# Performance work log

Measured on AMD Instinct MI355X. Metric: run time of the kernel, lower is better.

The kernel has to match this reference:

```python
import math
import jax, jax.numpy as jnp
import numpy as np

INPUT_DIM = 1024
OUTPUT_DIM = 1024
DEGREE = 8
EPS = 1.0


def setup_inputs() -> dict:
    key = jax.random.key(0)
    k1, k2 = jax.random.split(key)
    x = jax.random.normal(k1, (8192, INPUT_DIM), dtype=jnp.float32)
    std = 1.0 / (INPUT_DIM * (DEGREE + 1))
    hermite_coeffs = std * jax.random.normal(k2, (INPUT_DIM, OUTPUT_DIM, DEGREE + 1), dtype=jnp.float32)
    return {"x": x, "hermite_coeffs": hermite_coeffs}


def _hermite_basis(x):
    # x: [B, I] squashed input; returns [B, I, DEGREE+1] Hermite-function basis.
    pi_q = math.pi ** (-0.25)
    gauss = jnp.exp(-0.5 * x * x)
    h0 = pi_q * gauss
    hs = [h0]
    if DEGREE > 0:
        hs.append(math.sqrt(2.0) * pi_q * x * gauss)
    for i in range(2, DEGREE + 1):
        hs.append(math.sqrt(2.0 / i) * x * hs[i - 1] - math.sqrt((i - 1) / i) * hs[i - 2])
    return jnp.stack(hs, axis=-1)


def reference(x, hermite_coeffs):
    x = x.reshape(-1, INPUT_DIM)
    x = jnp.tanh(x) * (math.sqrt(2 * DEGREE + 1) + EPS)
    hermite = _hermite_basis(x)  # [B, I, D+1]
    y = jnp.einsum('bid,iod->bo', hermite, hermite_coeffs)
    return y.reshape(-1, OUTPUT_DIM)
```

## Files before the change

kernel.cpp:

```cpp
#include <hip/hip_runtime.h>

#define MDIM 8192
#define IDIM 1024
#define ODIM 1024
#define D1   9
#define KDIM (IDIM * D1)

typedef _Float16 half8   __attribute__((ext_vector_type(8)));
typedef _Float16 half2v  __attribute__((ext_vector_type(2)));
typedef float    float4v __attribute__((ext_vector_type(4)));

#define BSCALE 256.0f
#define INV_BSCALE (1.0f / 256.0f)
#define USCALE 5.123105625617661f
#define H0C 0.7511255444649425f
#define SQRT2 1.4142135623730951f

__device__ __forceinline__ void hermite9(float xv, float h[D1]) {
    float ax = fabsf(xv);
    float t  = __expf(-2.0f * ax);
    float th = (1.0f - t) / (1.0f + t);
    th = copysignf(th, xv);
    float u = th * USCALE;
    float g = __expf(-0.5f * u * u);
    h[0] = H0C * g;
    h[1] = SQRT2 * H0C * u * g;
    const float c1[D1] = {0.f, 0.f, 1.0f, 0.8164965809277260f, 0.7071067811865476f,
                          0.6324555320336759f, 0.5773502691896258f, 0.5345224838248488f, 0.5f};
    const float c2[D1] = {0.f, 0.f, 0.7071067811865476f, 0.8164965809277260f, 0.8660254037844386f,
                          0.8944271909999159f, 0.9128709291752769f, 0.9258200997725514f, 0.9354143466934853f};
#pragma unroll
    for (int d = 2; d < D1; ++d) h[d] = c1[d] * u * h[d - 1] - c2[d] * h[d - 2];
}

__global__ __launch_bounds__(256) void prep_b(const float* __restrict__ C,
                                              _Float16* __restrict__ Bt) {
    __shared__ float lds[288 * 33];
    const int t  = threadIdx.x;
    const int ti = blockIdx.x & 31;
    const int to = blockIdx.x >> 5;
    const float* base = C + (size_t)ti * 32 * 9216 + (size_t)to * 32 * 9;
#pragma unroll
    for (int j = 0; j < 36; ++j) {
        int f   = t + 256 * j;
        int row = f / 288;
        int col = f - row * 288;
        lds[col * 33 + row] = base[(size_t)row * 9216 + col];
    }
    __syncthreads();
    _Float16* bb = Bt + (size_t)to * 32 * KDIM + ti * 32;
#pragma unroll
    for (int j = 0; j < 36; ++j) {
        int e   = t + 256 * j;
        int i   = e & 31;
        int odp = e >> 5;
        int ol  = odp / 9;
        int d   = odp - ol * 9;
        bb[(size_t)ol * KDIM + d * IDIM + i] = (_Float16)(lds[odp * 33 + i] * BSCALE);
    }
}

__global__ __launch_bounds__(256) void prep_u(const float* __restrict__ x,
                                              _Float16* __restrict__ U,
                                              _Float16* __restrict__ H0) {
    size_t t = (size_t)blockIdx.x * 256 + threadIdx.x;
    const float4* xp = (const float4*)(x + t * 8);
    float4 a0 = xp[0], a1 = xp[1];
    float xv[8] = {a0.x, a0.y, a0.z, a0.w, a1.x, a1.y, a1.z, a1.w};
    half8 uu, hh;
#pragma unroll
    for (int e = 0; e < 8; ++e) {
        float v  = xv[e];
        float t2 = __expf(-2.0f * fabsf(v));
        float th = (1.0f - t2) / (1.0f + t2);
        float u  = copysignf(th, v) * USCALE;
        float g  = __expf(-0.5f * u * u);
        uu[e] = (_Float16)u;
        hh[e] = (_Float16)(H0C * g);
    }
    *(half8*)(U  + t * 8) = uu;
    *(half8*)(H0 + t * 8) = hh;
}

__global__ __launch_bounds__(256, 2) void gemm_fused3(
    const _Float16* __restrict__ U,
    const _Float16* __restrict__ H0,
    const _Float16* __restrict__ Bt,
    float* __restrict__ out)
{
    const int tid = threadIdx.x;
    const int w = tid >> 6;
    const int l = tid & 63;
    const int bn = blockIdx.x;
    const int bm = blockIdx.y;

    __shared__ _Float16 As[128 * 64];
    __shared__ _Float16 Bs[3][128 * 64];

    const int lrow8 = l >> 3;
    const int kgrp  = (l & 7) ^ lrow8;
    const _Float16* Bg = Bt + ((size_t)(bn * 128 + w * 8 + lrow8) * KDIM + kgrp * 8);

    const int q   = l >> 4;
    const int m16 = l & 15;
    const int s3  = m16 & 7;
    const int wm  = w >> 1, wn = w & 1;

    const int r  = tid >> 1;
    const int ih = tid & 1;
    const int r7 = r & 7;
    const size_t urow = (((size_t)(bm * 128 + r)) << 10) + ih * 32;

    constexpr float c1a[D1] = {0.f, 0.f, 1.0f, 0.8164965809277260f, 0.7071067811865476f,
                               0.6324555320336759f, 0.5773502691896258f, 0.5345224838248488f, 0.5f};
    constexpr float c2a[D1] = {0.f, 0.f, 0.7071067811865476f, 0.8164965809277260f, 0.8660254037844386f,
                               0.8944271909999159f, 0.9128709291752769f, 0.9258200997725514f, 0.9354143466934853f};

    half2v u2[16], hA[16], hB[16], ht[16];
    half8  ub[4], hb[4];
    const half2v sq2 = half2v{(_Float16)SQRT2, (_Float16)SQRT2};

    _Float16* arow = &As[r * 64];
    auto writeA = [&](const half2v* hts) {
#pragma unroll
        for (int c = 0; c < 4; ++c) {
            int slot = (ih * 4 + c) ^ r7;
            half8 vv;
#pragma unroll
            for (int pp = 0; pp < 4; ++pp) {
                vv[2*pp+0] = hts[4*c+pp][0];
                vv[2*pp+1] = hts[4*c+pp][1];
            }
            *(half8*)(arow + slot * 8) = vv;
        }
    };

    float4v acc[4][4] = {};

    {
        const half8* up = (const half8*)(U  + urow);
        const half8* hp = (const half8*)(H0 + urow);
#pragma unroll
        for (int a = 0; a < 4; ++a) { ub[a] = up[a]; hb[a] = hp[a]; }
#pragma unroll
        for (int a = 0; a < 4; ++a)
#pragma unroll
            for (int b = 0; b < 4; ++b) {
                u2[4*a+b] = half2v{ub[a][2*b], ub[a][2*b+1]};
                hA[4*a+b] = half2v{hb[a][2*b], hb[a][2*b+1]};
            }
#pragma unroll
        for (int p = 0; p < 16; ++p) { hB[p] = sq2 * u2[p] * hA[p]; ht[p] = hB[p]; }
    }
#pragma unroll
    for (int rr = 0; rr < 4; ++rr)
        __builtin_amdgcn_global_load_lds(
            (const __attribute__((address_space(1))) void*)(Bg + (size_t)(rr * 32) * KDIM),
            (__attribute__((address_space(3))) void*)((char*)&Bs[0][0] + (rr * 4 + w) * 1024),
            16, 0, 0);
#pragma unroll
    for (int rr = 0; rr < 4; ++rr)
        __builtin_amdgcn_global_load_lds(
            (const __attribute__((address_space(1))) void*)(Bg + (size_t)(rr * 32) * KDIM + IDIM),
            (__attribute__((address_space(3))) void*)((char*)&Bs[1][0] + (rr * 4 + w) * 1024),
            16, 0, 0);
    writeA(hA);
    asm volatile("s_waitcnt vmcnt(4) lgkmcnt(0)" ::: "memory");
    __builtin_amdgcn_s_barrier();
    asm volatile("" ::: "memory");

    auto window = [&](int ib, int d, bool do_e, bool do_wa, bool do_uh,
                      bool do_dma, int waitN, bool do_sync2, bool do_sync1) {
        const int cbuf = d % 3;

        __builtin_amdgcn_s_setprio(1);
#pragma unroll
        for (int ko = 0; ko < 2; ++ko) {
            const int slot = (q + 4 * ko) ^ s3;
            half8 af[4], bf[4];
#pragma unroll
            for (int i = 0; i < 4; ++i) {
                af[i] = *(const half8*)&As[(wm * 64 + i * 16 + m16) * 64 + slot * 8];
                bf[i] = *(const half8*)&Bs[cbuf][(wn * 64 + i * 16 + m16) * 64 + slot * 8];
            }
#pragma unroll
            for (int i = 0; i < 4; ++i)
#pragma unroll
                for (int j = 0; j < 4; ++j)
                    acc[i][j] = __builtin_amdgcn_mfma_f32_16x16x32_f16(af[i], bf[j], acc[i][j], 0, 0, 0);
        }
        __builtin_amdgcn_s_setprio(0);

        half2v htn[16];
        if (do_e) {
            const int t2d = (d <= 6) ? (d + 2) : (d - 7);
            if (t2d == 0) {
#pragma unroll
                for (int a = 0; a < 4; ++a)
#pragma unroll
                    for (int b = 0; b < 4; ++b) {
                        u2[4*a+b]  = half2v{ub[a][2*b], ub[a][2*b+1]};
                        htn[4*a+b] = half2v{hb[a][2*b], hb[a][2*b+1]};
                    }
#pragma unroll
                for (int p = 0; p < 16; ++p) hB[p] = htn[p];
            } else if (t2d == 1) {
#pragma unroll
                for (int p = 0; p < 16; ++p) {
                    htn[p] = sq2 * u2[p] * hB[p];
                    hA[p] = hB[p]; hB[p] = htn[p];
                }
            } else {
                const half2v c1v = half2v{(_Float16)c1a[t2d], (_Float16)c1a[t2d]};
                const half2v c2v = half2v{(_Float16)c2a[t2d], (_Float16)c2a[t2d]};
#pragma unroll
                for (int p = 0; p < 16; ++p) {
                    half2v tt = u2[p] * hB[p];
                    htn[p] = c1v * tt - c2v * hA[p];
                    hA[p] = hB[p]; hB[p] = htn[p];
                }
            }
        }

        if (do_sync2) {
            asm volatile("s_waitcnt lgkmcnt(0)" ::: "memory");
            __builtin_amdgcn_s_barrier();
            asm volatile("" ::: "memory");
        }

        if (do_wa) writeA(ht);
        if (do_e) {
#pragma unroll
            for (int p = 0; p < 16; ++p) ht[p] = htn[p];
        }
        if (do_uh) {
            const half8* up = (const half8*)(U  + urow + (size_t)(ib + 1) * 64);
            const half8* hp = (const half8*)(H0 + urow + (size_t)(ib + 1) * 64);
#pragma unroll
            for (int a = 0; a < 4; ++a) { ub[a] = up[a]; hb[a] = hp[a]; }
        }
        if (do_dma) {
            const int nkoff = (d <= 6) ? ((d + 2) * IDIM + ib * 64)
                                       : ((d - 7) * IDIM + ib * 64 + 64);
            const int nbuf = (d + 2) % 3;
#pragma unroll
            for (int rr = 0; rr < 4; ++rr)
                __builtin_amdgcn_global_load_lds(
                    (const __attribute__((address_space(1))) void*)(Bg + (size_t)(rr * 32) * KDIM + nkoff),
                    (__attribute__((address_space(3))) void*)((char*)&Bs[nbuf][0] + (rr * 4 + w) * 1024),
                    16, 0, 0);
        }
        if (do_sync1) {
            if (waitN == 12)     asm volatile("s_waitcnt vmcnt(12) lgkmcnt(0)" ::: "memory");
            else if (waitN == 4) asm volatile("s_waitcnt vmcnt(4) lgkmcnt(0)" ::: "memory");
            else                 asm volatile("s_waitcnt vmcnt(0) lgkmcnt(0)" ::: "memory");
            __builtin_amdgcn_s_barrier();
            asm volatile("" ::: "memory");
        }
    };

    for (int ib = 0; ib < 15; ++ib) {
#pragma unroll
        for (int d = 0; d < D1; ++d)
            window(ib, d, true, true, (d == 6), true, (d == 6) ? 12 : 4, true, true);
    }
    {
#pragma unroll
        for (int d = 0; d < 6; ++d)
            window(15, d, true, true, false, true, 4, true, true);
        window(15, 6, true,  true,  false, true,  4, true, true);
        window(15, 7, false, true,  false, false, 0, true, true);
        window(15, 8, false, false, false, false, 0, false, false);
    }

#pragma unroll
    for (int i = 0; i < 4; ++i) {
        int row = bm * 128 + wm * 64 + i * 16 + q * 4;
#pragma unroll
        for (int j = 0; j < 4; ++j) {
            int col = bn * 128 + wn * 64 + j * 16 + m16;
            float* op = out + (size_t)row * ODIM + col;
#pragma unroll
            for (int r2 = 0; r2 < 4; ++r2)
                op[(size_t)r2 * ODIM] = acc[i][j][r2] * INV_BSCALE;
        }
    }
}

__global__ void naive_kernel(const float* __restrict__ x, const float* __restrict__ C,
                             float* __restrict__ out) {
    __shared__ float hb[IDIM * D1];
    int b = blockIdx.x;
    int tid = threadIdx.x;
    for (int i = tid; i < IDIM; i += 256) {
        float h[D1];
        hermite9(x[(size_t)b * IDIM + i], h);
#pragma unroll
        for (int d = 0; d < D1; ++d) hb[i * D1 + d] = h[d];
    }
    __syncthreads();
    for (int o = tid; o < ODIM; o += 256) {
        float acc = 0.f;
        for (int i = 0; i < IDIM; ++i) {
            const float* cp = C + ((size_t)i * ODIM + o) * D1;
            const float* hp = hb + i * D1;
#pragma unroll
            for (int d = 0; d < D1; ++d) acc += hp[d] * cp[d];
        }
        out[(size_t)b * ODIM + o] = acc;
    }
}

extern "C" void kernel_launch(void* const* d_in, const int* in_sizes, int n_in,
                              void* d_out, int out_size, void* d_ws, size_t ws_size,
                              hipStream_t stream) {
    const float* x      = (const float*)d_in[0];
    const float* coeffs = (const float*)d_in[1];
    float* out = (float*)d_out;

    const size_t bt_bytes = (size_t)ODIM * KDIM * sizeof(_Float16);
    const size_t u_bytes  = (size_t)MDIM * IDIM * sizeof(_Float16);

    if (ws_size >= bt_bytes + 2 * u_bytes) {
        _Float16* Bt = (_Float16*)d_ws;
        _Float16* Uv = (_Float16*)((char*)d_ws + bt_bytes);
        _Float16* H0 = (_Float16*)((char*)d_ws + bt_bytes + u_bytes);
        hipLaunchKernelGGL(prep_b, dim3(1024), dim3(256), 0, stream, coeffs, Bt);
        hipLaunchKernelGGL(prep_u, dim3((MDIM * IDIM) / 2048), dim3(256), 0, stream, x, Uv, H0);
        hipLaunchKernelGGL(gemm_fused3, dim3(8, 64), dim3(256), 0, stream, Uv, H0, Bt, out);
    } else {
        hipLaunchKernelGGL(naive_kernel, dim3(MDIM), dim3(256), 0, stream, x, coeffs, out);
    }
}
```

Baseline: 274.0 us.

## Build Hermite A-fragments in registers instead of staging them through LDS

```diff
diff --git a/kernel.cpp b/kernel.cpp
--- a/kernel.cpp
+++ b/kernel.cpp
@@ -50,13 +50,19 @@
     __syncthreads();
     _Float16* bb = Bt + (size_t)to * 32 * KDIM + ti * 32;
 #pragma unroll
-    for (int j = 0; j < 36; ++j) {
-        int e   = t + 256 * j;
-        int i   = e & 31;
-        int odp = e >> 5;
-        int ol  = odp / 9;
-        int d   = odp - ol * 9;
-        bb[(size_t)ol * KDIM + d * IDIM + i] = (_Float16)(lds[odp * 33 + i] * BSCALE);
+    for (int j = 0; j < 5; ++j) {
+        int s = t + 256 * j;
+        if (s < 1152) {
+            int i8  = s & 3;
+            int odp = s >> 2;
+            int ol  = odp / 9;
+            int d   = odp - ol * 9;
+            half8 vv;
+#pragma unroll
+            for (int e = 0; e < 8; ++e)
+                vv[e] = (_Float16)(lds[odp * 33 + i8 * 8 + e] * BSCALE);
+            *(half8*)(bb + (size_t)ol * KDIM + d * IDIM + i8 * 8) = vv;
+        }
     }
 }
 
@@ -82,7 +88,7 @@
     *(half8*)(H0 + t * 8) = hh;
 }
 
-__global__ __launch_bounds__(256, 2) void gemm_fused3(
+__global__ __launch_bounds__(256, 2) void gemm_fused4(
     const _Float16* __restrict__ U,
     const _Float16* __restrict__ H0,
     const _Float16* __restrict__ Bt,
@@ -94,7 +100,6 @@
     const int bn = blockIdx.x;
     const int bm = blockIdx.y;
 
-    __shared__ _Float16 As[128 * 64];
     __shared__ _Float16 Bs[3][128 * 64];
 
     const int lrow8 = l >> 3;
@@ -106,154 +111,96 @@
     const int s3  = m16 & 7;
     const int wm  = w >> 1, wn = w & 1;
 
-    const int r  = tid >> 1;
-    const int ih = tid & 1;
-    const int r7 = r & 7;
-    const size_t urow = (((size_t)(bm * 128 + r)) << 10) + ih * 32;
+    const size_t ubase = ((size_t)(bm * 128 + wm * 64 + m16)) << 10;
 
     constexpr float c1a[D1] = {0.f, 0.f, 1.0f, 0.8164965809277260f, 0.7071067811865476f,
                                0.6324555320336759f, 0.5773502691896258f, 0.5345224838248488f, 0.5f};
     constexpr float c2a[D1] = {0.f, 0.f, 0.7071067811865476f, 0.8164965809277260f, 0.8660254037844386f,
                                0.8944271909999159f, 0.9128709291752769f, 0.9258200997725514f, 0.9354143466934853f};
 
-    half2v u2[16], hA[16], hB[16], ht[16];
-    half8  ub[4], hb[4];
-    const half2v sq2 = half2v{(_Float16)SQRT2, (_Float16)SQRT2};
-
-    _Float16* arow = &As[r * 64];
-    auto writeA = [&](const half2v* hts) {
-#pragma unroll
-        for (int c = 0; c < 4; ++c) {
-            int slot = (ih * 4 + c) ^ r7;
-            half8 vv;
-#pragma unroll
-            for (int pp = 0; pp < 4; ++pp) {
-                vv[2*pp+0] = hts[4*c+pp][0];
-                vv[2*pp+1] = hts[4*c+pp][1];
+    half8 u8[8], hA8[8], hB8[8];
+
+    auto loadUH = [&](int ib) {
+        const int ibo = ib * 64;
+#pragma unroll
+        for (int i16 = 0; i16 < 4; ++i16)
+#pragma unroll
+            for (int ko = 0; ko < 2; ++ko) {
+                const size_t off = ubase + ((size_t)(i16 * 16) << 10) + ibo + (q + 4 * ko) * 8;
+                u8 [i16 * 2 + ko] = *(const half8*)(U  + off);
+                hA8[i16 * 2 + ko] = *(const half8*)(H0 + off);
             }
-            *(half8*)(arow + slot * 8) = vv;
-        }
     };
 
+    auto dmaB = [&](int nkoff, int nbuf) {
+#pragma unroll
+        for (int rr = 0; rr < 4; ++rr)
+            __builtin_amdgcn_global_load_lds(
+                (const __attribute__((address_space(1))) void*)(Bg + (size_t)(rr * 32) * KDIM + nkoff),
+                (__attribute__((address_space(3))) void*)((char*)&Bs[nbuf][0] + (rr * 4 + w) * 1024),
+                16, 0, 0);
+    };
+
     float4v acc[4][4] = {};
 
-    {
-        const half8* up = (const half8*)(U  + urow);
-        const half8* hp = (const half8*)(H0 + urow);
-#pragma unroll
-        for (int a = 0; a < 4; ++a) { ub[a] = up[a]; hb[a] = hp[a]; }
-#pragma unroll
-        for (int a = 0; a < 4; ++a)
-#pragma unroll
-            for (int b = 0; b < 4; ++b) {
-                u2[4*a+b] = half2v{ub[a][2*b], ub[a][2*b+1]};
-                hA[4*a+b] = half2v{hb[a][2*b], hb[a][2*b+1]};
-            }
-#pragma unroll
-        for (int p = 0; p < 16; ++p) { hB[p] = sq2 * u2[p] * hA[p]; ht[p] = hB[p]; }
-    }
-#pragma unroll
-    for (int rr = 0; rr < 4; ++rr)
-        __builtin_amdgcn_global_load_lds(
-            (const __attribute__((address_space(1))) void*)(Bg + (size_t)(rr * 32) * KDIM),
-            (__attribute__((address_space(3))) void*)((char*)&Bs[0][0] + (rr * 4 + w) * 1024),
-            16, 0, 0);
-#pragma unroll
-    for (int rr = 0; rr < 4; ++rr)
-        __builtin_amdgcn_global_load_lds(
-            (const __attribute__((address_space(1))) void*)(Bg + (size_t)(rr * 32) * KDIM + IDIM),
-            (__attribute__((address_space(3))) void*)((char*)&Bs[1][0] + (rr * 4 + w) * 1024),
-            16, 0, 0);
-    writeA(hA);
-    asm volatile("s_waitcnt vmcnt(4) lgkmcnt(0)" ::: "memory");
+    loadUH(0);
+    dmaB(0, 0);
+    dmaB(IDIM, 1);
+    asm volatile("s_waitcnt vmcnt(4)" ::: "memory");
     __builtin_amdgcn_s_barrier();
     asm volatile("" ::: "memory");
 
-    auto window = [&](int ib, int d, bool do_e, bool do_wa, bool do_uh,
-                      bool do_dma, int waitN, bool do_sync2, bool do_sync1) {
+    auto window = [&](int ib, int d, bool do_uh, bool do_dma, int waitN, bool do_sync) {
         const int cbuf = d % 3;
+
+        if (do_uh) loadUH(ib + 1);
 
         __builtin_amdgcn_s_setprio(1);
 #pragma unroll
         for (int ko = 0; ko < 2; ++ko) {
             const int slot = (q + 4 * ko) ^ s3;
-            half8 af[4], bf[4];
+            half8 bf[4];
+#pragma unroll
+            for (int j = 0; j < 4; ++j)
+                bf[j] = *(const half8*)&Bs[cbuf][(wn * 64 + j * 16 + m16) * 64 + slot * 8];
 #pragma unroll
             for (int i = 0; i < 4; ++i) {
-                af[i] = *(const half8*)&As[(wm * 64 + i * 16 + m16) * 64 + slot * 8];
-                bf[i] = *(const half8*)&Bs[cbuf][(wn * 64 + i * 16 + m16) * 64 + slot * 8];
+                half8 af = (d == 0) ? hA8[i * 2 + ko] : hB8[i * 2 + ko];
+#pragma unroll
+                for (int j = 0; j < 4; ++j)
+                    acc[i][j] = __builtin_amdgcn_mfma_f32_16x16x32_f16(af, bf[j], acc[i][j], 0, 0, 0);
             }
-#pragma unroll
-            for (int i = 0; i < 4; ++i)
-#pragma unroll
-                for (int j = 0; j < 4; ++j)
-                    acc[i][j] = __builtin_amdgcn_mfma_f32_16x16x32_f16(af[i], bf[j], acc[i][j], 0, 0, 0);
         }
         __builtin_amdgcn_s_setprio(0);
 
-        half2v htn[16];
-        if (do_e) {
-            const int t2d = (d <= 6) ? (d + 2) : (d - 7);
-            if (t2d == 0) {
-#pragma unroll
-                for (int a = 0; a < 4; ++a)
-#pragma unroll
-                    for (int b = 0; b < 4; ++b) {
-                        u2[4*a+b]  = half2v{ub[a][2*b], ub[a][2*b+1]};
-                        htn[4*a+b] = half2v{hb[a][2*b], hb[a][2*b+1]};
-                    }
-#pragma unroll
-                for (int p = 0; p < 16; ++p) hB[p] = htn[p];
-            } else if (t2d == 1) {
-#pragma unroll
-                for (int p = 0; p < 16; ++p) {
-                    htn[p] = sq2 * u2[p] * hB[p];
-                    hA[p] = hB[p]; hB[p] = htn[p];
-                }
-            } else {
-                const half2v c1v = half2v{(_Float16)c1a[t2d], (_Float16)c1a[t2d]};
-                const half2v c2v = half2v{(_Float16)c2a[t2d], (_Float16)c2a[t2d]};
-#pragma unroll
-                for (int p = 0; p < 16; ++p) {
-                    half2v tt = u2[p] * hB[p];
-                    htn[p] = c1v * tt - c2v * hA[p];
-                    hA[p] = hB[p]; hB[p] = htn[p];
-                }
+        if (d == 0) {
+            const _Float16 s2 = (_Float16)SQRT2;
+            half8 s2v = {s2, s2, s2, s2, s2, s2, s2, s2};
+#pragma unroll
+            for (int p = 0; p < 8; ++p) hB8[p] = s2v * u8[p] * hA8[p];
+        } else if (d <= 7) {
+            const _Float16 c1 = (_Float16)c1a[d + 1];
+            const _Float16 c2 = (_Float16)c2a[d + 1];
+            half8 c1v = {c1, c1, c1, c1, c1, c1, c1, c1};
+            half8 c2v = {c2, c2, c2, c2, c2, c2, c2, c2};
+#pragma unroll
+            for (int p = 0; p < 8; ++p) {
+                half8 tt = u8[p] * hB8[p];
+                half8 ht = c1v * tt - c2v * hA8[p];
+                hA8[p] = hB8[p];
+                hB8[p] = ht;
             }
         }
 
-        if (do_sync2) {
-            asm volatile("s_waitcnt lgkmcnt(0)" ::: "memory");
-            __builtin_amdgcn_s_barrier();
-            asm volatile("" ::: "memory");
-        }
-
-        if (do_wa) writeA(ht);
-        if (do_e) {
-#pragma unroll
-            for (int p = 0; p < 16; ++p) ht[p] = htn[p];
-        }
-        if (do_uh) {
-            const half8* up = (const half8*)(U  + urow + (size_t)(ib + 1) * 64);
-            const half8* hp = (const half8*)(H0 + urow + (size_t)(ib + 1) * 64);
-#pragma unroll
-            for (int a = 0; a < 4; ++a) { ub[a] = up[a]; hb[a] = hp[a]; }
-        }
         if (do_dma) {
             const int nkoff = (d <= 6) ? ((d + 2) * IDIM + ib * 64)
                                        : ((d - 7) * IDIM + ib * 64 + 64);
-            const int nbuf = (d + 2) % 3;
-#pragma unroll
-            for (int rr = 0; rr < 4; ++rr)
-                __builtin_amdgcn_global_load_lds(
-                    (const __attribute__((address_space(1))) void*)(Bg + (size_t)(rr * 32) * KDIM + nkoff),
-                    (__attribute__((address_space(3))) void*)((char*)&Bs[nbuf][0] + (rr * 4 + w) * 1024),
-                    16, 0, 0);
-        }
-        if (do_sync1) {
-            if (waitN == 12)     asm volatile("s_waitcnt vmcnt(12) lgkmcnt(0)" ::: "memory");
-            else if (waitN == 4) asm volatile("s_waitcnt vmcnt(4) lgkmcnt(0)" ::: "memory");
-            else                 asm volatile("s_waitcnt vmcnt(0) lgkmcnt(0)" ::: "memory");
+            dmaB(nkoff, (d + 2) % 3);
+        }
+
+        if (do_sync) {
+            if (waitN == 4) asm volatile("s_waitcnt vmcnt(4) lgkmcnt(0)" ::: "memory");
+            else            asm volatile("s_waitcnt vmcnt(0) lgkmcnt(0)" ::: "memory");
             __builtin_amdgcn_s_barrier();
             asm volatile("" ::: "memory");
         }
@@ -262,15 +209,14 @@
     for (int ib = 0; ib < 15; ++ib) {
 #pragma unroll
         for (int d = 0; d < D1; ++d)
-            window(ib, d, true, true, (d == 6), true, (d == 6) ? 12 : 4, true, true);
+            window(ib, d,  (d == 8),  true,  4,  true);
     }
     {
 #pragma unroll
-        for (int d = 0; d < 6; ++d)
-            window(15, d, true, true, false, true, 4, true, true);
-        window(15, 6, true,  true,  false, true,  4, true, true);
-        window(15, 7, false, true,  false, false, 0, true, true);
-        window(15, 8, false, false, false, false, 0, false, false);
+        for (int d = 0; d < 7; ++d)
+            window(15, d, false, true, 4, true);
+        window(15, 7, false, false, 0, true);
+        window(15, 8, false, false, 0, false);
     }
 
 #pragma unroll
@@ -327,7 +273,7 @@
         _Float16* H0 = (_Float16*)((char*)d_ws + bt_bytes + u_bytes);
         hipLaunchKernelGGL(prep_b, dim3(1024), dim3(256), 0, stream, coeffs, Bt);
         hipLaunchKernelGGL(prep_u, dim3((MDIM * IDIM) / 2048), dim3(256), 0, stream, x, Uv, H0);
-        hipLaunchKernelGGL(gemm_fused3, dim3(8, 64), dim3(256), 0, stream, Uv, H0, Bt, out);
+        hipLaunchKernelGGL(gemm_fused4, dim3(8, 64), dim3(256), 0, stream, Uv, H0, Bt, out);
     } else {
         hipLaunchKernelGGL(naive_kernel, dim3(MDIM), dim3(256), 0, stream, x, coeffs, out);
     }
```

New measurement: 274.7 us. Within noise of the previous version (+0.2%).
